# Kernel optimization log

Hardware: AMD Instinct MI355X
Metric: run time of the kernel (lower is better)

## Reference

```python
import jax, jax.numpy as jnp
import numpy as np

HEADS = 8
CONTEXT_FRAMES = 128
REL_POS_MAX = 128


def setup_inputs() -> dict:
    key = jax.random.key(0)
    ks = jax.random.split(key, 6)
    b, c, f, t = 2, 512, 64, 512
    x = jax.random.normal(ks[0], (b, c, f, t), dtype=jnp.float32)
    # Linear weights stored as [in, out] (equivalent to torch weight.T)
    W_qkv = jax.random.normal(ks[1], (c, 3 * c), dtype=jnp.float32) * (c ** -0.5)
    b_qkv = jnp.zeros((3 * c,), dtype=jnp.float32)
    W_proj = jax.random.normal(ks[2], (c, c), dtype=jnp.float32) * (c ** -0.5)
    b_proj = jnp.zeros((c,), dtype=jnp.float32)
    rel_pos_bias = jax.random.normal(ks[3], (HEADS, REL_POS_MAX), dtype=jnp.float32) * 0.02
    return {"x": x, "W_qkv": W_qkv, "b_qkv": b_qkv, "W_proj": W_proj,
            "b_proj": b_proj, "rel_pos_bias": rel_pos_bias}


def reference(x, W_qkv, b_qkv, W_proj, b_proj, rel_pos_bias):
    b, c, f, t = x.shape
    hd = c // HEADS
    # (b, c, f, t) -> (b*f, t, c)
    h = jnp.transpose(x, (0, 2, 3, 1)).reshape(b * f, t, c)
    qkv = (h @ W_qkv + b_qkv).reshape(b * f, t, 3, HEADS, hd)
    q, k, v = qkv[:, :, 0], qkv[:, :, 1], qkv[:, :, 2]  # [bf, t, H, hd]
    scale = hd ** -0.5
    scores = jnp.einsum('nqhd,nkhd->nhqk', q, k) * scale  # [bf, H, t, t]
    # causal band mask + gathered relative-position bias
    dist = jnp.arange(t)[:, None] - jnp.arange(t)[None, :]  # [t, t]
    invalid = (dist < 0) | (dist >= CONTEXT_FRAMES)
    bias = rel_pos_bias[:, jnp.clip(dist, 0, REL_POS_MAX - 1)]  # [H, t, t]
    scores = scores + bias[None]
    scores = jnp.where(invalid[None, None], -jnp.inf, scores)
    attn = jax.nn.softmax(scores, axis=-1)
    y = jnp.einsum('nhqk,nkhd->nqhd', attn, v).reshape(b * f, t, c)
    y = y @ W_proj + b_proj
    return jnp.transpose(y.reshape(b, f, t, c), (0, 3, 1, 2))
```

## Files before the change

### kernel.cpp

```cpp
#include <hip/hip_runtime.h>
#include <hip/hip_bf16.h>

typedef short s16x8 __attribute__((ext_vector_type(8)));
typedef unsigned short u16x4 __attribute__((ext_vector_type(4)));
typedef float f32x4 __attribute__((ext_vector_type(4)));

#define MFMA16(a,b,c) __builtin_amdgcn_mfma_f32_16x16x32_bf16((a),(b),(c),0,0,0)

__device__ __forceinline__ unsigned short f2bf(float x){
  unsigned int u = __float_as_uint(x);
  u += 0x7fffu + ((u >> 16) & 1u);
  return (unsigned short)(u >> 16);
}

__device__ __forceinline__ void gl_lds16(const unsigned short* g, unsigned short* l){
  __builtin_amdgcn_global_load_lds((const __attribute__((address_space(1))) unsigned int*)g,
                                   (__attribute__((address_space(3))) unsigned int*)l, 16, 0, 0);
}

__global__ void __launch_bounds__(256) wt_prep(const float* __restrict__ Wq, const float* __restrict__ Wp,
                                               unsigned short* __restrict__ WqT, unsigned short* __restrict__ WpT){
  const int idx = blockIdx.x*256 + threadIdx.x;
  if (idx < 786432){
    const int nn = idx >> 9, kk = idx & 511;
    WqT[idx] = f2bf(Wq[kk*1536 + nn]);
  } else {
    const int i2 = idx - 786432;
    const int nn = i2 >> 9, kk = i2 & 511;
    WpT[i2] = f2bf(Wp[kk*512 + nn]);
  }
}

__global__ void __launch_bounds__(256) x_to_h(const float* __restrict__ x, unsigned short* __restrict__ h){
  __shared__ unsigned short tb[64][65];
  const int blk = blockIdx.x;
  const int ttt = blk & 7, cht = (blk >> 3) & 7, n = blk >> 6;
  const int b = n >> 6, f = n & 63;
  const int t = threadIdx.x;
  const int tt0 = ttt*64, ch0 = cht*64;
  const float* xb = x + ((size_t)(b*512 + ch0)*64 + f)*512 + tt0;
  const int ttl = t & 63;
  #pragma unroll
  for (int it = 0; it < 16; ++it){
    const int chl = it*4 + (t >> 6);
    tb[chl][ttl] = f2bf(xb[(size_t)chl*32768 + ttl]);
  }
  __syncthreads();
  unsigned short* hb = h + ((size_t)n*512 + tt0)*512 + ch0;
  const int c2 = (t & 31)*2;
  #pragma unroll
  for (int it = 0; it < 8; ++it){
    const int ttw = it*8 + (t >> 5);
    unsigned int v = (unsigned int)tb[c2][ttw] | ((unsigned int)tb[c2+1][ttw] << 16);
    *(unsigned int*)(hb + (size_t)ttw*512 + c2) = v;
  }
}

__device__ __forceinline__ void gemm_core_128(const unsigned short* __restrict__ A,
                                              const unsigned short* __restrict__ Bt,
                                              char* smem, int bm, int bn, int tid,
                                              f32x4 (&acc)[4][4]){
  const int lane = tid & 63, w = tid >> 6;
  const int wr = w >> 1, wc = w & 1;
  const int glog = (lane & 7) ^ ((lane >> 3) & 7);
  const unsigned short* Ab = A  + (size_t)(bm*128 + w*32 + (lane>>3))*512 + glog*8;
  const unsigned short* Bb = Bt + (size_t)(bn*128 + w*32 + (lane>>3))*512 + glog*8;
  unsigned short* AsW = (unsigned short*)smem + w*2048;
  unsigned short* BsW = (unsigned short*)(smem + 16384) + w*2048;
  const int rowoff = (lane & 15)*128;
  const int axor = lane & 7;
  const int ag = lane >> 4;
  for (int kt = 0; kt < 8; ++kt){
    const unsigned short* Ag = Ab + kt*64;
    const unsigned short* Bg = Bb + kt*64;
    gl_lds16(Ag          , AsW);
    gl_lds16(Ag +  8*512 , AsW + 512);
    gl_lds16(Ag + 16*512 , AsW + 1024);
    gl_lds16(Ag + 24*512 , AsW + 1536);
    gl_lds16(Bg          , BsW);
    gl_lds16(Bg +  8*512 , BsW + 512);
    gl_lds16(Bg + 16*512 , BsW + 1024);
    gl_lds16(Bg + 24*512 , BsW + 1536);
    __syncthreads();
    #pragma unroll
    for (int ks = 0; ks < 2; ++ks){
      s16x8 av[4], bv[4];
      const int g16 = ((ks*4 + ag) ^ axor) * 16;
      #pragma unroll
      for (int i = 0; i < 4; ++i){
        av[i] = *(const s16x8*)(smem +         (wr*64 + i*16)*128 + rowoff + g16);
        bv[i] = *(const s16x8*)(smem + 16384 + (wc*64 + i*16)*128 + rowoff + g16);
      }
      #pragma unroll
      for (int i = 0; i < 4; ++i)
        #pragma unroll
        for (int j = 0; j < 4; ++j)
          acc[i][j] = MFMA16(av[i], bv[j], acc[i][j]);
    }
    __syncthreads();
  }
}

__global__ void __launch_bounds__(256) qkv_gemm(const unsigned short* __restrict__ h,
                                                const unsigned short* __restrict__ WqT,
                                                const float* __restrict__ bqkv,
                                                unsigned short* __restrict__ Qb,
                                                unsigned short* __restrict__ Kb,
                                                unsigned short* __restrict__ Vt){
  __shared__ __align__(16) char smem[34816];
  const int tid = threadIdx.x;
  const int bm = blockIdx.x / 12, bn = blockIdx.x % 12;
  f32x4 acc[4][4] = {};
  gemm_core_128(h, WqT, smem, bm, bn, tid, acc);
  const int lane = tid & 63, w = tid >> 6, wr = w >> 1, wc = w & 1;
  const int c0 = bn * 128;
  float bj[4];
  #pragma unroll
  for (int j = 0; j < 4; ++j) bj[j] = bqkv[c0 + wc*64 + j*16 + (lane & 15)];
  unsigned short* Cs = (unsigned short*)smem;
  #pragma unroll
  for (int i = 0; i < 4; ++i)
    #pragma unroll
    for (int j = 0; j < 4; ++j)
      #pragma unroll
      for (int r = 0; r < 4; ++r){
        const int row = wr*64 + i*16 + (lane>>4)*4 + r;
        const int col = wc*64 + j*16 + (lane & 15);
        Cs[row*136 + col] = f2bf(acc[i][j][r] + bj[j]);
      }
  __syncthreads();
  const int n = bm >> 2, tt0 = (bm & 3) * 128;
  const int sel = bn >> 2, cq0 = (bn & 3) * 128;
  if (sel < 2){
    unsigned short* dst = (sel == 0) ? Qb : Kb;
    #pragma unroll
    for (int it = 0; it < 8; ++it){
      const int idx = it*256 + tid;
      const int row = idx >> 4, colc = (idx & 15)*8;
      const int cq = cq0 + colc, head = cq >> 6, d0 = cq & 63;
      s16x8 v = *(const s16x8*)(Cs + row*136 + colc);
      *(s16x8*)(dst + ((size_t)(n*8 + head)*512 + tt0 + row)*64 + d0) = v;
    }
  } else {
    const int col = tid >> 1;
    const int cq = cq0 + col, head = cq >> 6, d = cq & 63;
    #pragma unroll
    for (int it = 0; it < 8; ++it){
      const int ttl0 = (it*2 + (tid & 1))*8;
      s16x8 v;
      #pragma unroll
      for (int r = 0; r < 8; ++r) v[r] = (short)Cs[(ttl0 + r)*136 + col];
      *(s16x8*)(Vt + ((size_t)(n*8 + head)*64 + d)*512 + tt0 + ttl0) = v;
    }
  }
}

__global__ void __launch_bounds__(256) attn_kernel(const unsigned short* __restrict__ Qb,
                                                   const unsigned short* __restrict__ Kb,
                                                   const unsigned short* __restrict__ Vt,
                                                   const float* __restrict__ relb,
                                                   unsigned short* __restrict__ ys){
  __shared__ float biasS[128];
  __shared__ __align__(16) unsigned short P[4][16*72];
  const int blk = blockIdx.x;
  const int qb = blk & 7, hh = (blk >> 3) & 7, n = blk >> 6;
  const int tid = threadIdx.x, lane = tid & 63, w = tid >> 6;
  if (tid < 128) biasS[tid] = relb[hh*128 + tid];
  __syncthreads();
  const int q0 = qb*64, qw0 = q0 + w*16;
  const size_t nh = (size_t)(n*8 + hh);
  const int lq = lane & 15, lg = lane >> 4;
  const unsigned short* Qp = Qb + (nh*512 + qw0 + lq)*64 + lg*8;
  s16x8 bq0 = *(const s16x8*)(Qp);
  s16x8 bq1 = *(const s16x8*)(Qp + 32);
  f32x4 yacc[4] = {};
  float m_run = -INFINITY, l_run = 0.f;
  const int qg = qw0 + lq;
  unsigned short* Pw = P[w];
  for (int kt = 0; kt < 3; ++kt){
    const int kt0 = q0 - 128 + kt*64;
    if (kt0 < 0) continue;
    f32x4 s[4] = {};
    const unsigned short* Kp = Kb + (nh*512 + kt0 + lq)*64 + lg*8;
    #pragma unroll
    for (int mk = 0; mk < 4; ++mk){
      s16x8 kv0 = *(const s16x8*)(Kp + mk*1024);
      s16x8 kv1 = *(const s16x8*)(Kp + mk*1024 + 32);
      s[mk] = MFMA16(kv0, bq0, s[mk]);
      s[mk] = MFMA16(kv1, bq1, s[mk]);
    }
    float pmax = -3.0e38f;
    float sv[4][4];
    #pragma unroll
    for (int mk = 0; mk < 4; ++mk)
      #pragma unroll
      for (int r = 0; r < 4; ++r){
        const int kkl = mk*16 + lg*4 + r;
        const int dist = qg - (kt0 + kkl);
        float xv;
        if (dist >= 0 && dist < 128) xv = s[mk][r]*0.125f + biasS[dist];
        else                         xv = -1.0e30f;
        sv[mk][r] = xv;
        pmax = fmaxf(pmax, xv);
      }
    pmax = fmaxf(pmax, __shfl_xor(pmax, 16, 64));
    pmax = fmaxf(pmax, __shfl_xor(pmax, 32, 64));
    const float m_new = fmaxf(m_run, pmax);
    const float scalef = __expf(m_run - m_new);
    float psum = 0.f;
    #pragma unroll
    for (int mk = 0; mk < 4; ++mk){
      u16x4 pk;
      #pragma unroll
      for (int r = 0; r < 4; ++r){
        const float pe = __expf(sv[mk][r] - m_new);
        psum += pe;
        pk[r] = f2bf(pe);
      }
      *(u16x4*)(Pw + lq*72 + mk*16 + lg*4) = pk;
    }
    psum += __shfl_xor(psum, 16, 64);
    psum += __shfl_xor(psum, 32, 64);
    l_run = l_run*scalef + psum;
    m_run = m_new;
    #pragma unroll
    for (int i = 0; i < 4; ++i) yacc[i] *= scalef;
    const unsigned short* Vp = Vt + (nh*64 + lq)*512 + kt0 + lg*8;
    #pragma unroll
    for (int ks2 = 0; ks2 < 2; ++ks2){
      s16x8 pb = *(const s16x8*)(Pw + lq*72 + ks2*32 + lg*8);
      #pragma unroll
      for (int i = 0; i < 4; ++i){
        s16x8 vv = *(const s16x8*)(Vp + i*8192 + ks2*32);
        yacc[i] = MFMA16(vv, pb, yacc[i]);
      }
    }
  }
  const float inv = 1.f / l_run;
  unsigned short* yp = ys + ((size_t)n*512 + qw0 + lq)*512 + hh*64 + lg*4;
  #pragma unroll
  for (int i = 0; i < 4; ++i){
    u16x4 o;
    #pragma unroll
    for (int r = 0; r < 4; ++r) o[r] = f2bf(yacc[i][r]*inv);
    *(u16x4*)(yp + i*16) = o;
  }
}

__global__ void __launch_bounds__(256) proj_gemm(const unsigned short* __restrict__ ys,
                                                 const unsigned short* __restrict__ WpT,
                                                 const float* __restrict__ bproj,
                                                 float* __restrict__ out){
  __shared__ __align__(16) char smem[34816];
  const int tid = threadIdx.x;
  const int bm = blockIdx.x >> 2, bn = blockIdx.x & 3;
  f32x4 acc[4][4] = {};
  gemm_core_128(ys, WpT, smem, bm, bn, tid, acc);
  const int lane = tid & 63, w = tid >> 6, wr = w >> 1, wc = w & 1;
  const int c0 = bn * 128;
  float bj[4];
  #pragma unroll
  for (int j = 0; j < 4; ++j) bj[j] = bproj[c0 + wc*64 + j*16 + (lane & 15)];
  float* Cs = (float*)smem;
  const int n = bm >> 2, b = n >> 6, f = n & 63, tt0 = (bm & 3)*128;
  #pragma unroll
  for (int p = 0; p < 2; ++p){
    __syncthreads();
    if (wr == p){
      #pragma unroll
      for (int i = 0; i < 4; ++i)
        #pragma unroll
        for (int j = 0; j < 4; ++j)
          #pragma unroll
          for (int r = 0; r < 4; ++r){
            const int rowl = i*16 + (lane>>4)*4 + r;
            const int col = wc*64 + j*16 + (lane & 15);
            Cs[rowl*133 + col] = acc[i][j][r] + bj[j];
          }
    }
    __syncthreads();
    #pragma unroll
    for (int it = 0; it < 8; ++it){
      const int idx = it*256 + tid;
      const int chl = idx >> 4, tc = (idx & 15)*4;
      f32x4 v;
      #pragma unroll
      for (int r = 0; r < 4; ++r) v[r] = Cs[(tc + r)*133 + chl];
      const int ch = c0 + chl;
      *(f32x4*)(out + ((size_t)(b*512 + ch)*64 + f)*512 + tt0 + p*64 + tc) = v;
    }
  }
}

extern "C" void kernel_launch(void* const* d_in, const int* in_sizes, int n_in,
                              void* d_out, int out_size, void* d_ws, size_t ws_size,
                              hipStream_t stream){
  const float* x     = (const float*)d_in[0];
  const float* Wqkv  = (const float*)d_in[1];
  const float* bqkv  = (const float*)d_in[2];
  const float* Wproj = (const float*)d_in[3];
  const float* bproj = (const float*)d_in[4];
  const float* relb  = (const float*)d_in[5];
  float* out = (float*)d_out;
  char* ws = (char*)d_ws;
  if (ws_size < (size_t)270532608) return;
  unsigned short* hbuf = (unsigned short*)(ws);
  unsigned short* Qb   = (unsigned short*)(ws + (size_t)67108864);
  unsigned short* Kb   = (unsigned short*)(ws + (size_t)134217728);
  unsigned short* Vt   = (unsigned short*)(ws + (size_t)201326592);
  unsigned short* WqT  = (unsigned short*)(ws + (size_t)268435456);
  unsigned short* WpT  = (unsigned short*)(ws + (size_t)270008320);

  hipLaunchKernelGGL(wt_prep,     dim3(4096), dim3(256), 0, stream, Wqkv, Wproj, WqT, WpT);
  hipLaunchKernelGGL(x_to_h,      dim3(8192), dim3(256), 0, stream, x, hbuf);
  hipLaunchKernelGGL(qkv_gemm,    dim3(6144), dim3(256), 0, stream, hbuf, WqT, bqkv, Qb, Kb, Vt);
  hipLaunchKernelGGL(attn_kernel, dim3(8192), dim3(256), 0, stream, Qb, Kb, Vt, relb, hbuf);
  hipLaunchKernelGGL(proj_gemm,   dim3(2048), dim3(256), 0, stream, hbuf, WpT, bproj, out);
}
```

Baseline: 444.2 us.

## Stage K/V tiles in LDS with double buffering; tile weight transpose

The attention kernel now handles 128 queries per block, with each wave owning 32 queries. K and V tiles are staged once per block into swizzled LDS using async global-to-LDS loads, double-buffered so the next tile loads during compute. This replaces the per-wave redundant global loads of K and V and cuts the grid in half. Separately, the weight transpose prep uses an LDS-tiled transpose so reads and writes are coalesced. The cost is more LDS per block and extra barriers, which may lower occupancy.

```diff
diff --git a/kernel.cpp b/kernel.cpp
--- a/kernel.cpp
+++ b/kernel.cpp
@@ -20,14 +20,30 @@
 
 __global__ void __launch_bounds__(256) wt_prep(const float* __restrict__ Wq, const float* __restrict__ Wp,
                                                unsigned short* __restrict__ WqT, unsigned short* __restrict__ WpT){
-  const int idx = blockIdx.x*256 + threadIdx.x;
-  if (idx < 786432){
-    const int nn = idx >> 9, kk = idx & 511;
-    WqT[idx] = f2bf(Wq[kk*1536 + nn]);
+  __shared__ unsigned short tb[64][65];
+  int blk = blockIdx.x;
+  const float* src; unsigned short* dst; int N, k0, n0;
+  if (blk < 192){
+    src = Wq; dst = WqT; N = 1536;
+    n0 = (blk % 24)*64; k0 = (blk / 24)*64;
   } else {
-    const int i2 = idx - 786432;
-    const int nn = i2 >> 9, kk = i2 & 511;
-    WpT[i2] = f2bf(Wp[kk*512 + nn]);
+    blk -= 192; src = Wp; dst = WpT; N = 512;
+    n0 = (blk & 7)*64; k0 = (blk >> 3)*64;
+  }
+  const int tid = threadIdx.x;
+  const int nl = tid & 63;
+  #pragma unroll
+  for (int it = 0; it < 16; ++it){
+    const int kl = it*4 + (tid >> 6);
+    tb[kl][nl] = f2bf(src[(size_t)(k0+kl)*N + n0 + nl]);
+  }
+  __syncthreads();
+  const int c2 = (tid & 31)*2;
+  #pragma unroll
+  for (int it = 0; it < 8; ++it){
+    const int nw = it*8 + (tid >> 5);
+    unsigned int v = (unsigned int)tb[c2][nw] | ((unsigned int)tb[c2+1][nw] << 16);
+    *(unsigned int*)(dst + (size_t)(n0+nw)*512 + k0 + c2) = v;
   }
 }
 
@@ -160,90 +176,151 @@
                                                    const unsigned short* __restrict__ Vt,
                                                    const float* __restrict__ relb,
                                                    unsigned short* __restrict__ ys){
+  __shared__ __align__(16) unsigned short KsL[2][4096];
+  __shared__ __align__(16) unsigned short VsL[2][4096];
+  __shared__ __align__(16) unsigned short P[4][2][16*72];
   __shared__ float biasS[128];
-  __shared__ __align__(16) unsigned short P[4][16*72];
   const int blk = blockIdx.x;
-  const int qb = blk & 7, hh = (blk >> 3) & 7, n = blk >> 6;
+  const int qt = blk & 3, hh = (blk >> 2) & 7, n = blk >> 5;
   const int tid = threadIdx.x, lane = tid & 63, w = tid >> 6;
   if (tid < 128) biasS[tid] = relb[hh*128 + tid];
-  __syncthreads();
-  const int q0 = qb*64, qw0 = q0 + w*16;
+  const int q0 = qt * 128;
   const size_t nh = (size_t)(n*8 + hh);
+  const unsigned short* Kbase = Kb + nh*32768;
+  const unsigned short* Vbase = Vt + nh*32768;
   const int lq = lane & 15, lg = lane >> 4;
-  const unsigned short* Qp = Qb + (nh*512 + qw0 + lq)*64 + lg*8;
-  s16x8 bq0 = *(const s16x8*)(Qp);
-  s16x8 bq1 = *(const s16x8*)(Qp + 32);
-  f32x4 yacc[4] = {};
-  float m_run = -INFINITY, l_run = 0.f;
-  const int qg = qw0 + lq;
-  unsigned short* Pw = P[w];
-  for (int kt = 0; kt < 3; ++kt){
+  const int qq0 = q0 + w*32;
+  s16x8 bq[2][2];
+  #pragma unroll
+  for (int qs = 0; qs < 2; ++qs){
+    const unsigned short* Qp = Qb + (nh*512 + qq0 + qs*16 + lq)*64 + lg*8;
+    bq[qs][0] = *(const s16x8*)(Qp);
+    bq[qs][1] = *(const s16x8*)(Qp + 32);
+  }
+  int r_[2], g_[2], dsl_[2];
+  #pragma unroll
+  for (int j = 0; j < 2; ++j){
+    const int slot = j*256 + w*64 + lane;
+    r_[j] = slot >> 3;
+    g_[j] = (slot & 7) ^ (r_[j] & 7);
+    dsl_[j] = (j*256 + w*64) * 8;
+  }
+  f32x4 yacc[2][4] = {{{0.f,0.f,0.f,0.f}}};
+  float m_run[2] = {-INFINITY, -INFINITY}, l_run[2] = {0.f, 0.f};
+  const int first = (q0 >= 128) ? 0 : ((128 - q0 + 63) >> 6);
+  int cur = 0;
+  {
+    const int kt0 = q0 - 128 + first*64;
+    #pragma unroll
+    for (int j = 0; j < 2; ++j){
+      gl_lds16(Kbase + (size_t)(kt0 + r_[j])*64 + g_[j]*8, KsL[0] + dsl_[j]);
+      gl_lds16(Vbase + (size_t)r_[j]*512 + kt0 + g_[j]*8,  VsL[0] + dsl_[j]);
+    }
+  }
+  for (int kt = first; kt < 4; ++kt){
     const int kt0 = q0 - 128 + kt*64;
-    if (kt0 < 0) continue;
-    f32x4 s[4] = {};
-    const unsigned short* Kp = Kb + (nh*512 + kt0 + lq)*64 + lg*8;
-    #pragma unroll
-    for (int mk = 0; mk < 4; ++mk){
-      s16x8 kv0 = *(const s16x8*)(Kp + mk*1024);
-      s16x8 kv1 = *(const s16x8*)(Kp + mk*1024 + 32);
-      s[mk] = MFMA16(kv0, bq0, s[mk]);
-      s[mk] = MFMA16(kv1, bq1, s[mk]);
-    }
-    float pmax = -3.0e38f;
-    float sv[4][4];
-    #pragma unroll
-    for (int mk = 0; mk < 4; ++mk)
-      #pragma unroll
-      for (int r = 0; r < 4; ++r){
-        const int kkl = mk*16 + lg*4 + r;
-        const int dist = qg - (kt0 + kkl);
-        float xv;
-        if (dist >= 0 && dist < 128) xv = s[mk][r]*0.125f + biasS[dist];
-        else                         xv = -1.0e30f;
-        sv[mk][r] = xv;
-        pmax = fmaxf(pmax, xv);
-      }
-    pmax = fmaxf(pmax, __shfl_xor(pmax, 16, 64));
-    pmax = fmaxf(pmax, __shfl_xor(pmax, 32, 64));
-    const float m_new = fmaxf(m_run, pmax);
-    const float scalef = __expf(m_run - m_new);
-    float psum = 0.f;
-    #pragma unroll
-    for (int mk = 0; mk < 4; ++mk){
-      u16x4 pk;
-      #pragma unroll
-      for (int r = 0; r < 4; ++r){
-        const float pe = __expf(sv[mk][r] - m_new);
-        psum += pe;
-        pk[r] = f2bf(pe);
-      }
-      *(u16x4*)(Pw + lq*72 + mk*16 + lg*4) = pk;
-    }
-    psum += __shfl_xor(psum, 16, 64);
-    psum += __shfl_xor(psum, 32, 64);
-    l_run = l_run*scalef + psum;
-    m_run = m_new;
-    #pragma unroll
-    for (int i = 0; i < 4; ++i) yacc[i] *= scalef;
-    const unsigned short* Vp = Vt + (nh*64 + lq)*512 + kt0 + lg*8;
-    #pragma unroll
-    for (int ks2 = 0; ks2 < 2; ++ks2){
-      s16x8 pb = *(const s16x8*)(Pw + lq*72 + ks2*32 + lg*8);
+    __syncthreads();
+    if (kt < 3){
+      const int nk0 = kt0 + 64;
+      #pragma unroll
+      for (int j = 0; j < 2; ++j){
+        gl_lds16(Kbase + (size_t)(nk0 + r_[j])*64 + g_[j]*8, KsL[cur^1] + dsl_[j]);
+        gl_lds16(Vbase + (size_t)r_[j]*512 + nk0 + g_[j]*8,  VsL[cur^1] + dsl_[j]);
+      }
+    }
+    const bool wact = (kt0 <= qq0 + 31);
+    if (wact){
+      s16x8 av[4][2];
+      #pragma unroll
+      for (int mk = 0; mk < 4; ++mk){
+        const int rr = mk*16 + lq;
+        const unsigned short* kp = KsL[cur] + rr*64;
+        av[mk][0] = *(const s16x8*)(kp + ((lg     ) ^ (rr & 7))*8);
+        av[mk][1] = *(const s16x8*)(kp + ((4 + lg ) ^ (rr & 7))*8);
+      }
+      float pex[2][4][4];
+      #pragma unroll
+      for (int qs = 0; qs < 2; ++qs){
+        const int qqs = qq0 + qs*16;
+        if (kt0 > qqs + 15 || kt0 + 63 < qqs - 127) continue;
+        f32x4 s4[4] = {{0.f,0.f,0.f,0.f}};
+        #pragma unroll
+        for (int mk = 0; mk < 4; ++mk){
+          s4[mk] = MFMA16(av[mk][0], bq[qs][0], s4[mk]);
+          s4[mk] = MFMA16(av[mk][1], bq[qs][1], s4[mk]);
+        }
+        const int qg = qqs + lq;
+        float pmax = -3.0e38f;
+        #pragma unroll
+        for (int mk = 0; mk < 4; ++mk)
+          #pragma unroll
+          for (int r = 0; r < 4; ++r){
+            const int dist = qg - (kt0 + mk*16 + lg*4 + r);
+            float xv;
+            if (dist >= 0 && dist < 128) xv = s4[mk][r]*0.125f + biasS[dist];
+            else                         xv = -1.0e30f;
+            pex[qs][mk][r] = xv;
+            pmax = fmaxf(pmax, xv);
+          }
+        pmax = fmaxf(pmax, __shfl_xor(pmax, 16, 64));
+        pmax = fmaxf(pmax, __shfl_xor(pmax, 32, 64));
+        const float m_new = fmaxf(m_run[qs], pmax);
+        const float scalef = __expf(m_run[qs] - m_new);
+        float psum = 0.f;
+        unsigned short* Pw = P[w][qs];
+        #pragma unroll
+        for (int mk = 0; mk < 4; ++mk){
+          u16x4 pk;
+          #pragma unroll
+          for (int r = 0; r < 4; ++r){
+            const float pe = __expf(pex[qs][mk][r] - m_new);
+            psum += pe;
+            pk[r] = f2bf(pe);
+          }
+          *(u16x4*)(Pw + lq*72 + mk*16 + lg*4) = pk;
+        }
+        psum += __shfl_xor(psum, 16, 64);
+        psum += __shfl_xor(psum, 32, 64);
+        l_run[qs] = l_run[qs]*scalef + psum;
+        m_run[qs] = m_new;
+        #pragma unroll
+        for (int i = 0; i < 4; ++i) yacc[qs][i] *= scalef;
+      }
+      s16x8 vv[4][2];
       #pragma unroll
       for (int i = 0; i < 4; ++i){
-        s16x8 vv = *(const s16x8*)(Vp + i*8192 + ks2*32);
-        yacc[i] = MFMA16(vv, pb, yacc[i]);
-      }
-    }
-  }
-  const float inv = 1.f / l_run;
-  unsigned short* yp = ys + ((size_t)n*512 + qw0 + lq)*512 + hh*64 + lg*4;
-  #pragma unroll
-  for (int i = 0; i < 4; ++i){
-    u16x4 o;
-    #pragma unroll
-    for (int r = 0; r < 4; ++r) o[r] = f2bf(yacc[i][r]*inv);
-    *(u16x4*)(yp + i*16) = o;
+        const int rr = i*16 + lq;
+        const unsigned short* vp = VsL[cur] + rr*64;
+        vv[i][0] = *(const s16x8*)(vp + ((lg    ) ^ (rr & 7))*8);
+        vv[i][1] = *(const s16x8*)(vp + ((4 + lg) ^ (rr & 7))*8);
+      }
+      #pragma unroll
+      for (int qs = 0; qs < 2; ++qs){
+        const int qqs = qq0 + qs*16;
+        if (kt0 > qqs + 15 || kt0 + 63 < qqs - 127) continue;
+        unsigned short* Pw = P[w][qs];
+        #pragma unroll
+        for (int ks2 = 0; ks2 < 2; ++ks2){
+          s16x8 pb = *(const s16x8*)(Pw + lq*72 + ks2*32 + lg*8);
+          #pragma unroll
+          for (int i = 0; i < 4; ++i)
+            yacc[qs][i] = MFMA16(vv[i][ks2], pb, yacc[qs][i]);
+        }
+      }
+    }
+    cur ^= 1;
+  }
+  #pragma unroll
+  for (int qs = 0; qs < 2; ++qs){
+    const float inv = 1.f / l_run[qs];
+    unsigned short* yp = ys + ((size_t)n*512 + qq0 + qs*16 + lq)*512 + hh*64 + lg*4;
+    #pragma unroll
+    for (int i = 0; i < 4; ++i){
+      u16x4 o;
+      #pragma unroll
+      for (int r = 0; r < 4; ++r) o[r] = f2bf(yacc[qs][i][r]*inv);
+      *(u16x4*)(yp + i*16) = o;
+    }
   }
 }
 
@@ -311,9 +388,9 @@
   unsigned short* WqT  = (unsigned short*)(ws + (size_t)268435456);
   unsigned short* WpT  = (unsigned short*)(ws + (size_t)270008320);
 
-  hipLaunchKernelGGL(wt_prep,     dim3(4096), dim3(256), 0, stream, Wqkv, Wproj, WqT, WpT);
+  hipLaunchKernelGGL(wt_prep,     dim3(256),  dim3(256), 0, stream, Wqkv, Wproj, WqT, WpT);
   hipLaunchKernelGGL(x_to_h,      dim3(8192), dim3(256), 0, stream, x, hbuf);
   hipLaunchKernelGGL(qkv_gemm,    dim3(6144), dim3(256), 0, stream, hbuf, WqT, bqkv, Qb, Kb, Vt);
-  hipLaunchKernelGGL(attn_kernel, dim3(8192), dim3(256), 0, stream, Qb, Kb, Vt, relb, hbuf);
+  hipLaunchKernelGGL(attn_kernel, dim3(4096), dim3(256), 0, stream, Qb, Kb, Vt, relb, hbuf);
   hipLaunchKernelGGL(proj_gemm,   dim3(2048), dim3(256), 0, stream, hbuf, WpT, bproj, out);
 }
```

After: 386.5 us. -13.0%, faster.
